# Optimization experiments

Hardware: AMD Instinct MI355X
Metric: run time of the kernel (lower is better)

Reference implementation:

```python
import jax, jax.numpy as jnp
import numpy as np

B, C, H, W = 2, 32, 128, 128
P = 32                      # encoder patch size (== decoder_out_feat_size_final_linear -> empty up_tail)
D = 512                     # encoder dim == decoder dim (enc_to_dec = Identity)
HEADS, DHEAD = 8, 64
ENC_DEPTH = 4
FLIN, CUP = 32, 4
DI, DS, K, DTR, OUTCH = 32, 8, 4, 2, 20   # SS2D dims (c_in=32 hardcoded in module)


def _ln(x, g, b):
    m = x.mean(-1, keepdims=True)
    v = ((x - m) ** 2).mean(-1, keepdims=True)
    return (x - m) / jnp.sqrt(v + 1e-5) * g + b


def _attn(x, g, b, wqkv, wo, bo):
    Bb, N, _ = x.shape
    qkv = _ln(x, g, b) @ wqkv
    q, k, v = jnp.split(qkv, 3, axis=-1)
    sp = lambda t: t.reshape(Bb, N, HEADS, DHEAD).transpose(0, 2, 1, 3)
    q, k, v = sp(q), sp(k), sp(v)
    a = jax.nn.softmax(jnp.einsum('bhnd,bhmd->bhnm', q, k) * (DHEAD ** -0.5), axis=-1)
    o = jnp.einsum('bhnm,bhmd->bhnd', a, v).transpose(0, 2, 1, 3).reshape(Bb, N, HEADS * DHEAD)
    return o @ wo + bo


def _ff(x, g, b, w1, b1, w2, b2):
    return jax.nn.gelu(_ln(x, g, b) @ w1 + b1, approximate=False) @ w2 + b2


def _conv(x, w, b, groups=1):
    y = jax.lax.conv_general_dilated(x, w, (1, 1), 'SAME',
        dimension_numbers=('NCHW', 'OIHW', 'NCHW'), feature_group_count=groups)
    return y + b[None, :, None, None]


def _fft2c(x):
    x = jnp.fft.ifftshift(x, axes=(-2, -1))
    x = jnp.fft.fft2(x, axes=(-2, -1), norm='ortho')
    return jnp.fft.fftshift(x, axes=(-2, -1))


def _ifft2c(x):
    x = jnp.fft.ifftshift(x, axes=(-2, -1))
    x = jnp.fft.ifft2(x, axes=(-2, -1), norm='ortho')
    return jnp.fft.fftshift(x, axes=(-2, -1))


def setup_inputs():
    key = jax.random.key(0)
    it = iter(jax.random.split(key, 80))
    nk = lambda: next(it)
    rn = lambda shape, s=0.02: jax.random.normal(nk(), shape, jnp.float32) * s
    nh, nw = H // P, W // P
    N = nh * nw
    pd = P * P * C
    inp = {}
    inp['in_imgs'] = jax.random.normal(nk(), (B, C, H, W), jnp.float32)
    inp['in_ksp'] = rn((B, C, H, W), 0.01)
    inp['mask'] = (jax.random.uniform(nk(), (B, 1, H, W)) < 0.3).astype(jnp.float32)
    s = jax.random.normal(nk(), (B, C, H, W), jnp.float32)
    sc = s[:, 0::2] + 1j * s[:, 1::2]
    sc = sc / jnp.sqrt(jnp.sum(jnp.abs(sc) ** 2, axis=1, keepdims=True) + 1e-8)
    inp['sens'] = jnp.stack([sc.real, sc.imag], axis=2).reshape(B, C, H, W)
    # patch embedding: LayerNorm(pd) -> Linear(pd, D) -> LayerNorm(D)
    inp['pe_ln1_g'] = jnp.ones((pd,)); inp['pe_ln1_b'] = jnp.zeros((pd,))
    inp['pe_w'] = rn((pd, D)); inp['pe_b'] = jnp.zeros((D,))
    inp['pe_ln2_g'] = jnp.ones((D,)); inp['pe_ln2_b'] = jnp.zeros((D,))
    inp['pos_emb'] = rn((1, N, D))
    dep = ENC_DEPTH
    inp['enc_aln_g'] = jnp.ones((dep, D)); inp['enc_aln_b'] = jnp.zeros((dep, D))
    inp['enc_wqkv'] = rn((dep, D, 3 * HEADS * DHEAD)); inp['enc_wo'] = rn((dep, HEADS * DHEAD, D)); inp['enc_bo'] = jnp.zeros((dep, D))
    inp['enc_fln_g'] = jnp.ones((dep, D)); inp['enc_fln_b'] = jnp.zeros((dep, D))
    inp['enc_w1'] = rn((dep, D, 2048)); inp['enc_b1'] = jnp.zeros((dep, 2048))
    inp['enc_w2'] = rn((dep, 2048, D)); inp['enc_b2'] = jnp.zeros((dep, D))
    inp['enc_ng'] = jnp.ones((D,)); inp['enc_nb'] = jnp.zeros((D,))
    inp['dec_pos'] = rn((N, D))
    inp['dec_aln_g'] = jnp.ones((D,)); inp['dec_aln_b'] = jnp.zeros((D,))
    inp['dec_wqkv'] = rn((D, 3 * HEADS * DHEAD)); inp['dec_wo'] = rn((HEADS * DHEAD, D)); inp['dec_bo'] = jnp.zeros((D,))
    inp['dec_fln_g'] = jnp.ones((D,)); inp['dec_fln_b'] = jnp.zeros((D,))
    inp['dec_w1'] = rn((D, 3072)); inp['dec_b1'] = jnp.zeros((3072,))
    inp['dec_w2'] = rn((3072, D)); inp['dec_b2'] = jnp.zeros((D,))
    inp['dec_ng'] = jnp.ones((D,)); inp['dec_nb'] = jnp.zeros((D,))
    inp['fin_w'] = rn((D, CUP * FLIN * FLIN)); inp['fin_b'] = jnp.zeros((CUP * FLIN * FLIN,))
    # SS2D params
    inp['ss_in_w'] = rn((C, 2 * DI), 0.1); inp['ss_in_b'] = jnp.zeros((2 * DI,))
    inp['ss_conv_w'] = rn((DI, 1, 3, 3), 0.1); inp['ss_conv_b'] = jnp.zeros((DI,))
    inp['ss_xproj'] = rn((K, DI, DTR + 2 * DS), 0.1)
    inp['ss_dt_w'] = rn((K, DTR, DI), 0.5); inp['ss_dt_b'] = rn((K, DI), 0.1)
    inp['ss_Alog'] = jnp.log(jnp.tile(jnp.arange(1, DS + 1, dtype=jnp.float32), (K, DI, 1)))
    inp['ss_D'] = jnp.ones((K, DI))
    inp['ss_ln_g'] = jnp.ones((DI,)); inp['ss_ln_b'] = jnp.zeros((DI,))
    inp['ss_out_w'] = rn((DI, OUTCH), 0.1); inp['ss_out_b'] = jnp.zeros((OUTCH,))
    # RefinementBlock (in_ch = CUP + 32 + OUTCH = 56)
    inp['last_head_w'] = rn((64, CUP + C + OUTCH, 3, 3), 0.05); inp['last_head_b'] = jnp.zeros((64,))
    inp['res_w1'] = rn((3, 64, 64, 3, 3), 0.05); inp['res_b1'] = jnp.zeros((3, 64))
    inp['res_w2'] = rn((3, 64, 64, 3, 3), 0.05); inp['res_b2'] = jnp.zeros((3, 64))
    inp['last_tail_w'] = rn((2, 64, 3, 3), 0.05); inp['last_tail_b'] = jnp.zeros((2,))
    inp['dc_alpha'] = jnp.array(1.0, jnp.float32)
    return inp


def _forward(in_imgs, in_ksp, mask, sens, pe_ln1_g, pe_ln1_b, pe_w, pe_b, pe_ln2_g, pe_ln2_b, pos_emb, enc_aln_g, enc_aln_b, enc_wqkv, enc_wo, enc_bo, enc_fln_g, enc_fln_b, enc_w1, enc_b1, enc_w2, enc_b2, enc_ng, enc_nb, dec_pos, dec_aln_g, dec_aln_b, dec_wqkv, dec_wo, dec_bo, dec_fln_g, dec_fln_b, dec_w1, dec_b1, dec_w2, dec_b2, dec_ng, dec_nb, fin_w, fin_b, ss_in_w, ss_in_b, ss_conv_w, ss_conv_b, ss_xproj, ss_dt_w, ss_dt_b, ss_Alog, ss_D, ss_ln_g, ss_ln_b, ss_out_w, ss_out_b, last_head_w, last_head_b, res_w1, res_b1, res_w2, res_b2, last_tail_w, last_tail_b, dc_alpha):
    nh, nw = H // P, W // P
    N = nh * nw
    # patchify: bb cc (h p1) (w p2) -> bb (h w) (p1 p2 cc)
    pch = in_imgs.reshape(B, C, nh, P, nw, P).transpose(0, 2, 4, 3, 5, 1).reshape(B, N, P * P * C)
    t = _ln(pch, pe_ln1_g, pe_ln1_b) @ pe_w + pe_b
    t = _ln(t, pe_ln2_g, pe_ln2_b)
    t = t + pos_emb   # pool == 'mean'
    for i in range(ENC_DEPTH):
        t = _attn(t, enc_aln_g[i], enc_aln_b[i], enc_wqkv[i], enc_wo[i], enc_bo[i]) + t
        t = _ff(t, enc_fln_g[i], enc_fln_b[i], enc_w1[i], enc_b1[i], enc_w2[i], enc_b2[i]) + t
    t = _ln(t, enc_ng, enc_nb)
    # decoder transformer (depth 1); enc_to_dec is Identity
    d = t + dec_pos[None]
    d = _attn(d, dec_aln_g, dec_aln_b, dec_wqkv, dec_wo, dec_bo) + d
    d = _ff(d, dec_fln_g, dec_fln_b, dec_w1, dec_b1, dec_w2, dec_b2) + d
    d = _ln(d, dec_ng, dec_nb)
    lat = d @ fin_w + fin_b
    # bb (nh nw) (cc p1 p2) -> bb cc (nh p1) (nw p2); up_tail is empty (P == FLIN)
    x = lat.reshape(B, nh, nw, CUP, FLIN, FLIN).transpose(0, 3, 1, 4, 2, 5).reshape(B, CUP, H, W)
    # ---- SS2D: 4-directional selective scan over in_ksp ----
    L = H * W
    xz = jnp.einsum('bchw,ce->behw', in_ksp, ss_in_w) + ss_in_b[None, :, None, None]
    xs0, z = xz[:, :DI], xz[:, DI:]
    xs0 = jax.nn.silu(_conv(xs0, ss_conv_w, ss_conv_b, groups=DI))
    x_hw = xs0.reshape(B, DI, L)
    x_wh = xs0.transpose(0, 1, 3, 2).reshape(B, DI, L)
    xs = jnp.stack([x_hw, x_wh, x_hw[..., ::-1], x_wh[..., ::-1]], axis=1)   # (B,K,DI,L)
    dbl = jnp.einsum('bkdl,kdc->bkcl', xs, ss_xproj)
    dtr, Bm, Cm = dbl[:, :, :DTR], dbl[:, :, DTR:DTR + DS], dbl[:, :, DTR + DS:]
    dts = jax.nn.softplus(jnp.einsum('bkrl,krd->bkdl', dtr, ss_dt_w) + ss_dt_b[None, :, :, None])
    A = -jnp.exp(ss_Alog)
    a = jnp.exp(jnp.einsum('bkdl,kds->bklds', dts, A))         # transition per step
    bb = jnp.einsum('bkdl,bksl->bklds', dts * xs, Bm)          # input per step
    def comb(e1, e2):
        a1, b1 = e1; a2, b2 = e2
        return a1 * a2, a2 * b1 + b2
    _, hs = jax.lax.associative_scan(comb, (a, bb), axis=2)    # (B,K,L,DI,DS)
    ys = jnp.einsum('bklds,bksl->bkdl', hs, Cm) + ss_D[None, :, :, None] * xs
    yh = ys[:, 0] + ys[:, 2, :, ::-1]
    yw = ys[:, 1] + ys[:, 3, :, ::-1]
    y = yh + yw.reshape(B, DI, W, H).transpose(0, 1, 3, 2).reshape(B, DI, L)
    y = y.reshape(B, DI, H, W).transpose(0, 2, 3, 1)           # BHWC
    y = _ln(y, ss_ln_g, ss_ln_b) * jax.nn.silu(z.transpose(0, 2, 3, 1))
    out_ss = (y @ ss_out_w + ss_out_b).transpose(0, 3, 1, 2)   # (B,OUTCH,H,W)
    # ---- refinement ----
    lrelu = lambda v: jnp.where(v > 0, v, 0.2 * v)
    xc = jnp.concatenate([x, in_imgs, out_ss], axis=1)
    h0 = lrelu(_conv(xc, last_head_w, last_head_b))
    for i in range(3):
        h0 = lrelu(h0 + _conv(lrelu(_conv(h0, res_w1[i], res_b1[i])), res_w2[i], res_b2[i]))
    x_ri = _conv(h0, last_tail_w, last_tail_b)   # (B,2,H,W)
    # ---- data consistency ----
    x_c = (x_ri[:, 0] + 1j * x_ri[:, 1])[:, None]
    k_meas = (in_ksp[:, 0::2] + 1j * in_ksp[:, 1::2]) * 100.0   # k_scale_ratio
    s_c = sens[:, 0::2] + 1j * sens[:, 1::2]
    k_pred = _fft2c(s_c * x_c)
    k_dc = k_pred + mask * dc_alpha * (k_meas - k_pred)
    x_comb = jnp.sum(_ifft2c(k_dc) * jnp.conj(s_c), axis=1)
    out_ri = jnp.stack([x_comb.real, x_comb.imag], axis=1)
    return jnp.sqrt(out_ri[:, 0:1] ** 2 + out_ri[:, 1:2] ** 2 + 1e-12)


reference = _forward
```

## Files before the change

kernel.cpp:

```cpp
#include <hip/hip_runtime.h>

#define PI_F 3.14159265358979323846f

constexpr int L_ = 16384;
constexpr int PD_ = 32768;

__device__ __forceinline__ float sigmoidf_(float x){ return 1.f/(1.f+__expf(-x)); }
__device__ __forceinline__ float softplusf_(float x){ return x>20.f ? x : log1pf(__expf(x)); }
__device__ __forceinline__ float geluf_(float x){ return 0.5f*x*(1.f+erff(x*0.70710678118654752f)); }

__device__ __forceinline__ float2 block_reduce2(float s, float ss){
  __shared__ float r1[256], r2[256];
  int tid = threadIdx.x;
  r1[tid]=s; r2[tid]=ss; __syncthreads();
  for(int o=128;o>0;o>>=1){ if(tid<o){ r1[tid]+=r1[tid+o]; r2[tid]+=r2[tid+o]; } __syncthreads(); }
  float2 out; out.x=r1[0]; out.y=r2[0]; __syncthreads();
  return out;
}

__global__ __launch_bounds__(256) void k_pesum(const float* __restrict__ img, float* __restrict__ stats){
  int blk=blockIdx.x; int m=blk>>3, sl=blk&7;
  int b=m>>4, n=m&15, ih=n>>2, iw=n&3;
  int tid=threadIdx.x;
  const float* base=img+(size_t)b*32*L_;
  float s=0.f, ss=0.f;
  for (int i=tid;i<4096;i+=256){
    int j=sl*4096+i;
    int c=j>>10, p1=(j>>5)&31, p2=j&31;
    float v=base[(size_t)c*L_+(ih*32+p1)*128+iw*32+p2];
    s+=v; ss+=v*v;
  }
  float2 r=block_reduce2(s,ss);
  if (tid==0){ atomicAdd(&stats[m*2],r.x); atomicAdd(&stats[m*2+1],r.y); }
}

__global__ __launch_bounds__(256) void k_penorm(const float* __restrict__ img, const float* __restrict__ stats,
                                                const float* __restrict__ g, const float* __restrict__ bv,
                                                float* __restrict__ xn){
  int blk=blockIdx.x; int m=blk>>3, sl=blk&7;
  int b=m>>4, n=m&15, ih=n>>2, iw=n&3;
  int tid=threadIdx.x;
  const float* base=img+(size_t)b*32*L_;
  float mean=stats[m*2]/(float)PD_;
  float var =stats[m*2+1]/(float)PD_-mean*mean;
  float inv =1.f/sqrtf(var+1e-5f);
  for (int i=tid;i<4096;i+=256){
    int j=sl*4096+i;
    int c=j>>10, p1=(j>>5)&31, p2=j&31;
    float v=base[(size_t)c*L_+(ih*32+p1)*128+iw*32+p2];
    int k=(p1*32+p2)*32+c;
    xn[(size_t)m*PD_+k]=(v-mean)*inv*g[k]+bv[k];
  }
}

template<int KC, int MODE>
__global__ __launch_bounds__(256) void k_gemm_sk(const float* __restrict__ A, const float* __restrict__ Bw,
                                                 const float* __restrict__ bias, float* __restrict__ C,
                                                 int N, int K){
  __shared__ float As[32][KC];
  int tid=threadIdx.x, tx=tid&63, ty=tid>>6;
  int n = blockIdx.x*64+tx;
  int k0 = blockIdx.y*KC;
  for (int i=tid;i<32*KC;i+=256){
    int r=i/KC, c=i%KC;
    float v=A[(size_t)r*K + k0 + c];
    if (MODE==1) v=geluf_(v);
    As[r][c]=v;
  }
  __syncthreads();
  float acc[8]={0,0,0,0,0,0,0,0};
  for (int kk=0;kk<KC;kk+=4){
    float b0=Bw[(size_t)(k0+kk)*N+n],   b1=Bw[(size_t)(k0+kk+1)*N+n];
    float b2=Bw[(size_t)(k0+kk+2)*N+n], b3=Bw[(size_t)(k0+kk+3)*N+n];
    #pragma unroll
    for (int r=0;r<8;r++){
      const float4 a=*(const float4*)&As[ty*8+r][kk];
      acc[r]+=a.x*b0+a.y*b1+a.z*b2+a.w*b3;
    }
  }
  bool addb = (bias!=nullptr) && (blockIdx.y==0);
  #pragma unroll
  for (int r=0;r<8;r++){
    int m=ty*8+r;
    float v=acc[r]+(addb?bias[n]:0.f);
    if (MODE==2){
      int b=m>>4, ih=(m>>2)&3, iw=m&3;
      int cu=n>>10, f1=(n>>5)&31, f2=n&31;
      atomicAdd(&C[((size_t)(b*4+cu)*128+ih*32+f1)*128+iw*32+f2], v);
    } else {
      atomicAdd(&C[(size_t)m*N+n], v);
    }
  }
}

__global__ __launch_bounds__(256) void k_pe_post(float* __restrict__ t,
                                                 const float* __restrict__ g, const float* __restrict__ bv,
                                                 const float* __restrict__ pos){
  int m=blockIdx.x, tid=threadIdx.x;
  float v0 = t[m*512+tid];
  float v1 = t[m*512+256+tid];
  float2 r = block_reduce2(v0+v1, v0*v0+v1*v1);
  float mean=r.x/512.f, var=r.y/512.f-mean*mean, inv=1.f/sqrtf(var+1e-5f);
  int n = m&15;
  t[m*512+tid]     = (v0-mean)*inv*g[tid]+bv[tid]         + pos[n*512+tid];
  t[m*512+256+tid] = (v1-mean)*inv*g[256+tid]+bv[256+tid] + pos[n*512+256+tid];
}

__global__ __launch_bounds__(256) void k_ln_tok(const float* __restrict__ src, const float* __restrict__ g,
                                                const float* __restrict__ bv, float* __restrict__ dst){
  int m=blockIdx.x, tid=threadIdx.x;
  float v0=src[m*512+tid], v1=src[m*512+256+tid];
  float2 r=block_reduce2(v0+v1, v0*v0+v1*v1);
  float mean=r.x/512.f, var=r.y/512.f-mean*mean, inv=1.f/sqrtf(var+1e-5f);
  dst[m*512+tid]     =(v0-mean)*inv*g[tid]+bv[tid];
  dst[m*512+256+tid] =(v1-mean)*inv*g[256+tid]+bv[256+tid];
}

__global__ void k_addpos(const float* __restrict__ t, const float* __restrict__ pos, float* __restrict__ dst){
  int i = blockIdx.x*256+threadIdx.x;
  int m=i>>9, j=i&511;
  dst[i]=t[i]+pos[(m&15)*512+j];
}

__global__ __launch_bounds__(256) void k_attn(const float* __restrict__ qkv, float* __restrict__ outb){
  int bh=blockIdx.x, b=bh>>3, h=bh&7, tid=threadIdx.x;
  __shared__ float q[16][64], kk[16][64], vv[16][64], pp[16][16];
  for (int i=tid;i<1024;i+=256){
    int row=i>>6, d=i&63;
    const float* src=qkv + (size_t)(b*16+row)*1536 + h*64+d;
    q[row][d]=src[0]; kk[row][d]=src[512]; vv[row][d]=src[1024];
  }
  __syncthreads();
  int i=tid>>4, j=tid&15;
  float s=0.f;
  #pragma unroll
  for (int d=0;d<64;d++) s+=q[i][d]*kk[j][d];
  s*=0.125f;
  float mx=s;
  for (int o=8;o>0;o>>=1) mx=fmaxf(mx,__shfl_xor(mx,o,16));
  float e=__expf(s-mx), sm=e;
  for (int o=8;o>0;o>>=1) sm+=__shfl_xor(sm,o,16);
  pp[i][j]=e/sm;
  __syncthreads();
  int d=tid&63;
  for (int pass=0;pass<4;pass++){
    int row=pass*4+(tid>>6);
    float acc=0.f;
    #pragma unroll
    for (int jj=0;jj<16;jj++) acc+=pp[row][jj]*vv[jj][d];
    outb[(size_t)(b*16+row)*512 + h*64+d]=acc;
  }
}

__global__ __launch_bounds__(256) void k_xz(const float* __restrict__ ksp, const float* __restrict__ w,
                                            const float* __restrict__ bv, float* __restrict__ xz){
  int blk=blockIdx.x; int b=blk>>6; int p0=(blk&63)*256; int tid=threadIdx.x;
  __shared__ float lin[32][256];
  __shared__ float lw[2048];
  for (int i=tid;i<2048;i+=256) lw[i]=w[i];
  for (int i=tid;i<8192;i+=256){ int c=i>>8, p=i&255; lin[c][p]=ksp[(size_t)(b*32+c)*L_+p0+p]; }
  __syncthreads();
  float xv[32];
  #pragma unroll
  for (int c=0;c<32;c++) xv[c]=lin[c][tid];
  for (int e=0;e<64;e++){
    float a=bv[e];
    #pragma unroll
    for (int c=0;c<32;c++) a+=xv[c]*lw[c*64+e];
    xz[(size_t)(b*64+e)*L_+p0+tid]=a;
  }
}

__global__ void k_dwconv(const float* __restrict__ xz, const float* __restrict__ w,
                         const float* __restrict__ bv, float* __restrict__ xs0){
  int i=blockIdx.x*256+threadIdx.x;
  int p=i&16383; int d=(i>>14)&31; int b=i>>19;
  int h=p>>7, ww=p&127;
  const float* src=xz+(size_t)(b*64+d)*L_;
  float acc=bv[d];
  for (int ky=0;ky<3;ky++){
    int hh=h+ky-1; if(hh<0||hh>127) continue;
    for (int kx=0;kx<3;kx++){
      int wx=ww+kx-1; if(wx<0||wx>127) continue;
      acc+=src[hh*128+wx]*w[d*9+ky*3+kx];
    }
  }
  xs0[(size_t)(b*32+d)*L_+p]=acc*sigmoidf_(acc);
}

__global__ __launch_bounds__(256) void k_transpose(const float* __restrict__ src, float* __restrict__ dst){
  __shared__ float tile[32][33];
  int z=blockIdx.z;
  int h0=blockIdx.y*32, w0=blockIdx.x*32;
  int tid=threadIdx.x, tx=tid&31, ty=tid>>5;
  const float* s=src+(size_t)z*L_;
  float* d=dst+(size_t)z*L_;
  for (int r=ty;r<32;r+=8) tile[r][tx]=s[(h0+r)*128+w0+tx];
  __syncthreads();
  for (int r=ty;r<32;r+=8) d[(w0+r)*128+h0+tx]=tile[tx][r];
}

__global__ __launch_bounds__(256) void k_dbl(const float* __restrict__ xs0, const float* __restrict__ xs0T,
                                             const float* __restrict__ xproj, float* __restrict__ dbl){
  int bk=blockIdx.y; int b=bk>>2, k=bk&3;
  int l0=blockIdx.x*256, tid=threadIdx.x;
  const float* src=(k&1)?xs0T:xs0;
  __shared__ float xv[32][256];
  __shared__ float xp[576];
  for (int i=tid;i<576;i+=256) xp[i]=xproj[k*576+i];
  for (int i=tid;i<8192;i+=256){
    int dd=i>>8, p=i&255; int l=l0+p; int li=(k<2)?l:(16383-l);
    xv[dd][p]=src[(size_t)(b*32+dd)*L_+li];
  }
  __syncthreads();
  float xr[32];
  #pragma unroll
  for (int dd=0;dd<32;dd++) xr[dd]=xv[dd][tid];
  float* out=&dbl[((size_t)(b*4+k)*L_ + l0+tid)*18];
  for (int c=0;c<18;c++){
    float a=0.f;
    #pragma unroll
    for (int dd=0;dd<32;dd++) a+=xr[dd]*xp[dd*18+c];
    out[c]=a;
  }
}

__global__ __launch_bounds__(256) void k_scan1(const float* __restrict__ dbl, const float* __restrict__ xs0,
                                               const float* __restrict__ xs0T, const float* __restrict__ dtw,
                                               const float* __restrict__ dtb, const float* __restrict__ Alog,
                                               float2* __restrict__ sm){
  int blk=blockIdx.x; int bk=blk>>7, c=blk&127;
  int b=bk>>2, k=bk&3;
  int tid=threadIdx.x, d=tid>>3, s=tid&7;
  __shared__ float ed[128][18];
  __shared__ float2 du[32][129];
  const float* dbase=dbl+((size_t)bk*L_+c*128)*18;
  for (int i=tid;i<2304;i+=256) ((float*)ed)[i]=dbase[i];
  __syncthreads();
  const float* src=(k&1)?xs0T:xs0;
  bool rev=(k>=2);
  for (int i=tid;i<4096;i+=256){
    int dd=i>>7, j=i&127; int l=c*128+j;
    float xsv=src[(size_t)(b*32+dd)*L_+(rev?(16383-l):l)];
    float w0=dtw[(k*2+0)*32+dd], w1=dtw[(k*2+1)*32+dd], bb=dtb[k*32+dd];
    float dt=softplusf_(ed[j][0]*w0+ed[j][1]*w1+bb);
    du[dd][j]=make_float2(dt, dt*xsv);
  }
  __syncthreads();
  float Av=-__expf(Alog[(k*32+d)*8+s]);
  float P=1.f, Q=0.f;
  for (int j=0;j<128;j++){
    float2 v=du[d][j];
    float a=__expf(v.x*Av);
    Q=a*Q+v.y*ed[j][2+s];
    P*=a;
  }
  sm[((size_t)bk*128+c)*256+tid]=make_float2(P,Q);
}

__global__ __launch_bounds__(256) void k_scan2(const float2* __restrict__ sm, float* __restrict__ pre){
  int bk=blockIdx.x, tid=threadIdx.x;
  float run=0.f;
  for (int cb=0; cb<128; cb+=16){
    float2 v[16];
    #pragma unroll
    for (int t=0;t<16;t++) v[t]=sm[((size_t)bk*128+cb+t)*256+tid];
    #pragma unroll
    for (int t=0;t<16;t++){
      pre[((size_t)bk*128+cb+t)*256+tid]=run;
      run=v[t].x*run+v[t].y;
    }
  }
}

__global__ __launch_bounds__(256) void k_scan3(const float* __restrict__ dbl, const float* __restrict__ xs0,
                                               const float* __restrict__ xs0T, const float* __restrict__ dtw,
                                               const float* __restrict__ dtb, const float* __restrict__ Alog,
                                               const float* __restrict__ pre, float* __restrict__ ys){
  int blk=blockIdx.x; int bk=blk>>7, c=blk&127;
  int b=bk>>2, k=bk&3;
  int tid=threadIdx.x, d=tid>>3, s=tid&7;
  __shared__ float ed[128][18];
  __shared__ float2 du[32][129];
  const float* dbase=dbl+((size_t)bk*L_+c*128)*18;
  for (int i=tid;i<2304;i+=256) ((float*)ed)[i]=dbase[i];
  __syncthreads();
  const float* src=(k&1)?xs0T:xs0;
  bool rev=(k>=2);
  for (int i=tid;i<4096;i+=256){
    int dd=i>>7, j=i&127; int l=c*128+j;
    float xsv=src[(size_t)(b*32+dd)*L_+(rev?(16383-l):l)];
    float w0=dtw[(k*2+0)*32+dd], w1=dtw[(k*2+1)*32+dd], bb=dtb[k*32+dd];
    float dt=softplusf_(ed[j][0]*w0+ed[j][1]*w1+bb);
    du[dd][j]=make_float2(dt, dt*xsv);
  }
  __syncthreads();
  float Av=-__expf(Alog[(k*32+d)*8+s]);
  float h=pre[((size_t)bk*128+c)*256+tid];
  float* yout=ys+((size_t)bk*32+d)*L_+c*128;
  for (int j=0;j<128;j++){
    float2 v=du[d][j];
    float a=__expf(v.x*Av);
    h=a*h+v.y*ed[j][2+s];
    float yp=h*ed[j][10+s];
    yp+=__shfl_xor(yp,1,8);
    yp+=__shfl_xor(yp,2,8);
    yp+=__shfl_xor(yp,4,8);
    if (s==0) yout[j]=yp;
  }
}

__global__ __launch_bounds__(256) void k_ycomb(const float* __restrict__ ys, const float* __restrict__ xz,
                                               const float* __restrict__ xs0, const float* __restrict__ Dp,
                                               const float* __restrict__ g, const float* __restrict__ bv,
                                               const float* __restrict__ ow, const float* __restrict__ ob,
                                               float* __restrict__ oss){
  int blk=blockIdx.x; int b=blk>>7; int pg=blk&127;
  int tid=threadIdx.x; int pos=tid&127; int team=tid>>7;
  int p=pg*128+pos;
  int lt=pos*128+pg;
  __shared__ float lw[640]; __shared__ float lb[20]; __shared__ float lg[32], lbv[32], lD[32];
  __shared__ float red[2][2][128];
  __shared__ float prj[128][21];
  for (int i=tid;i<640;i+=256) lw[i]=ow[i];
  if (tid<20) lb[tid]=ob[tid];
  if (tid<32){ lg[tid]=g[tid]; lbv[tid]=bv[tid]; lD[tid]=Dp[tid]+Dp[32+tid]+Dp[64+tid]+Dp[96+tid]; }
  __syncthreads();
  size_t base=(size_t)b*128*L_;
  int d0=team*16;
  float y[16];
  float s=0.f, ss=0.f;
  #pragma unroll
  for (int dd=0;dd<16;dd++){
    int d=d0+dd;
    float v=ys[base+(size_t)(0*32+d)*L_+p] + ys[base+(size_t)(2*32+d)*L_+16383-p]
          + ys[base+(size_t)(1*32+d)*L_+lt] + ys[base+(size_t)(3*32+d)*L_+16383-lt]
          + lD[d]*xs0[(size_t)(b*32+d)*L_+p];
    y[dd]=v; s+=v; ss+=v*v;
  }
  red[team][0][pos]=s; red[team][1][pos]=ss;
  __syncthreads();
  float S=red[0][0][pos]+red[1][0][pos];
  float SS=red[0][1][pos]+red[1][1][pos];
  float mean=S/32.f, var=SS/32.f-mean*mean, inv=1.f/sqrtf(var+1e-5f);
  float pc[20];
  #pragma unroll
  for (int c2=0;c2<20;c2++) pc[c2]=0.f;
  #pragma unroll
  for (int dd=0;dd<16;dd++){
    int d=d0+dd;
    float yn=(y[dd]-mean)*inv*lg[d]+lbv[d];
    float zv=xz[(size_t)(b*64+32+d)*L_+p];
    float t2=yn*(zv*sigmoidf_(zv));
    #pragma unroll
    for (int c2=0;c2<20;c2++) pc[c2]+=t2*lw[d*20+c2];
  }
  if (team==1){
    #pragma unroll
    for (int c2=0;c2<20;c2++) prj[pos][c2]=pc[c2];
  }
  __syncthreads();
  if (team==0){
    #pragma unroll
    for (int c2=0;c2<20;c2++) oss[(size_t)(b*20+c2)*L_+p]=lb[c2]+pc[c2]+prj[pos][c2];
  }
}

__global__ void k_concat(const float* __restrict__ x, const float* __restrict__ img,
                         const float* __restrict__ oss, float* __restrict__ xc){
  int i=blockIdx.x*256+threadIdx.x;
  int p=i&16383; int ch=(i>>14)%56; int b=i/(56*16384);
  float v;
  if (ch<4) v=x[(size_t)(b*4+ch)*L_+p];
  else if (ch<36) v=img[(size_t)(b*32+ch-4)*L_+p];
  else v=oss[(size_t)(b*20+ch-36)*L_+p];
  xc[i]=v;
}

template<int NCO>
__global__ __launch_bounds__(256) void k_conv3s(const float* __restrict__ in, const float* __restrict__ wt,
                                                float* __restrict__ sc, int Cin, int Cout, int CIS){
  int tile=blockIdx.x; int th0=(tile>>2)*32, tw0=(tile&3)*32;
  int cg=blockIdx.y;
  int bz=blockIdx.z; int b=bz>>1, ks=bz&1;
  int cibase=ks*CIS;
  int cic=Cin-cibase; if (cic>CIS) cic=CIS;
  __shared__ float wlds[32][NCO][9];
  __shared__ float ibuf[2][34][34];
  int tid=threadIdx.x;
  for (int i=tid;i<cic*NCO*9;i+=256){
    int ci=i/(NCO*9), rem=i%(NCO*9), co=rem/9, q=rem%9;
    wlds[ci][co][q]=wt[(((size_t)(cg*NCO+co))*Cin + cibase+ci)*9+q];
  }
  auto stage=[&](int buf, int ci){
    const float* src=in+((size_t)b*Cin+cibase+ci)*L_;
    for (int i=tid;i<34*34;i+=256){
      int r=i/34, c=i%34;
      int gh=th0+r-1, gw=tw0+c-1;
      ibuf[buf][r][c]=(gh>=0&&gh<128&&gw>=0&&gw<128)?src[gh*128+gw]:0.f;
    }
  };
  stage(0,0);
  __syncthreads();
  float acc[NCO][4];
  #pragma unroll
  for (int co=0;co<NCO;co++){acc[co][0]=0.f;acc[co][1]=0.f;acc[co][2]=0.f;acc[co][3]=0.f;}
  int tr=((tid>>4)&15)<<1, tc=(tid&15)<<1;
  for (int ci=0;ci<cic;ci++){
    int cur=ci&1;
    if (ci+1<cic) stage(cur^1, ci+1);
    float iv[4][4];
    #pragma unroll
    for (int dr=0;dr<4;dr++)
      #pragma unroll
      for (int dc=0;dc<4;dc++) iv[dr][dc]=ibuf[cur][tr+dr][tc+dc];
    #pragma unroll
    for (int co=0;co<NCO;co++){
      float w0=wlds[ci][co][0],w1=wlds[ci][co][1],w2=wlds[ci][co][2];
      float w3=wlds[ci][co][3],w4=wlds[ci][co][4],w5=wlds[ci][co][5];
      float w6=wlds[ci][co][6],w7=wlds[ci][co][7],w8=wlds[ci][co][8];
      acc[co][0]+=iv[0][0]*w0+iv[0][1]*w1+iv[0][2]*w2
                 +iv[1][0]*w3+iv[1][1]*w4+iv[1][2]*w5
                 +iv[2][0]*w6+iv[2][1]*w7+iv[2][2]*w8;
      acc[co][1]+=iv[0][1]*w0+iv[0][2]*w1+iv[0][3]*w2
                 +iv[1][1]*w3+iv[1][2]*w4+iv[1][3]*w5
                 +iv[2][1]*w6+iv[2][2]*w7+iv[2][3]*w8;
      acc[co][2]+=iv[1][0]*w0+iv[1][1]*w1+iv[1][2]*w2
                 +iv[2][0]*w3+iv[2][1]*w4+iv[2][2]*w5
                 +iv[3][0]*w6+iv[3][1]*w7+iv[3][2]*w8;
      acc[co][3]+=iv[1][1]*w0+iv[1][2]*w1+iv[1][3]*w2
                 +iv[2][1]*w3+iv[2][2]*w4+iv[2][3]*w5
                 +iv[3][1]*w6+iv[3][2]*w7+iv[3][3]*w8;
    }
    __syncthreads();
  }
  #pragma unroll
  for (int co=0;co<NCO;co++){
    int gco=cg*NCO+co;
    float* dst=sc+((size_t)((ks*2+b)*Cout+gco))*L_+(size_t)(th0+tr)*128+tw0+tc;
    float2 a={acc[co][0],acc[co][1]}, c={acc[co][2],acc[co][3]};
    *(float2*)dst=a;
    *(float2*)(dst+128)=c;
  }
}

__global__ void k_epi(const float* __restrict__ sc, const float* __restrict__ bias,
                      const float* __restrict__ res, float* __restrict__ out, int Cout, int act){
  int i=blockIdx.x*256+threadIdx.x;
  int co=(i/L_)%Cout;
  size_t half=(size_t)2*Cout*L_;
  float v=sc[i]+sc[half+i]+bias[co];
  if (res) v+=res[i];
  if (act) v=v>0.f?v:0.2f*v;
  out[i]=v;
}

__device__ __forceinline__ int rev7(int x){
  return ((x&1)<<6)|((x&2)<<4)|((x&4)<<2)|(x&8)|((x&16)>>2)|((x&32)>>4)|((x&64)>>6);
}

__global__ __launch_bounds__(256) void k_fftA(const float* __restrict__ x_ri, const float* __restrict__ sens,
                                              float* __restrict__ tmp){
  int blk=blockIdx.x; int b=blk>>7, coil=(blk>>3)&15, rg=blk&7;
  int r0=rg*16;
  __shared__ float Ar[16][128], Ai[16][128];
  __shared__ float twr[64], twi[64];
  int tid=threadIdx.x;
  if (tid<64){ float ang=-2.f*PI_F*(float)tid/128.f; twr[tid]=cosf(ang); twi[tid]=sinf(ang); }
  const float* srp=sens+(size_t)(b*32+2*coil)*L_;
  const float* sip=sens+(size_t)(b*32+2*coil+1)*L_;
  const float* xrp=x_ri+(size_t)(b*2)*L_;
  const float* xip=xrp+L_;
  for (int i=tid;i<2048;i+=256){
    int lr=i>>7, w=i&127; int gh=r0+lr; int idx=gh*128+w;
    float sg=((gh+w)&1)?-1.f:1.f;
    float sr=srp[idx],si=sip[idx],xr=xrp[idx],xi=xip[idx];
    Ar[lr][w]=sg*(sr*xr-si*xi);
    Ai[lr][w]=sg*(sr*xi+si*xr);
  }
  __syncthreads();
  for (int s=0;s<7;s++){
    int m=64>>s;
    for (int q=tid;q<1024;q+=256){
      int lr=q>>6, jj=q&63;
      int j=jj&(m-1), gg=jj>>(6-s);
      int kpos=(gg<<(7-s))+j;
      int tw=j<<s;
      float ur=Ar[lr][kpos],ui=Ai[lr][kpos],vr=Ar[lr][kpos+m],vi=Ai[lr][kpos+m];
      Ar[lr][kpos]=ur+vr; Ai[lr][kpos]=ui+vi;
      float dr=ur-vr,di=ui-vi,wr=twr[tw],wi=twi[tw];
      Ar[lr][kpos+m]=dr*wr-di*wi; Ai[lr][kpos+m]=dr*wi+di*wr;
    }
    __syncthreads();
  }
  float* tr=tmp+(size_t)(b*16+coil)*2*L_;
  float* ti=tr+L_;
  for (int i=tid;i<2048;i+=256){
    int lr=i>>7, w=i&127; int idx=(r0+lr)*128+w;
    tr[idx]=Ar[lr][w]; ti[idx]=Ai[lr][w];
  }
}

__global__ __launch_bounds__(256) void k_fftB(float* __restrict__ tmp, const float* __restrict__ ksp,
                                              const float* __restrict__ mask, const float* __restrict__ alpha_p){
  int blk=blockIdx.x; int b=blk>>7, coil=(blk>>3)&15, cg=blk&7;
  int c0=cg*16;
  __shared__ float Br[128][17], Bi[128][17];
  __shared__ float twr[64], twi[64];
  int tid=threadIdx.x;
  if (tid<64){ float ang=-2.f*PI_F*(float)tid/128.f; twr[tid]=cosf(ang); twi[tid]=sinf(ang); }
  float* tr=tmp+(size_t)(b*16+coil)*2*L_;
  float* ti=tr+L_;
  for (int i=tid;i<2048;i+=256){
    int r=i>>4, lc=i&15;
    Br[r][lc]=tr[r*128+c0+lc]; Bi[r][lc]=ti[r*128+c0+lc];
  }
  __syncthreads();
  for (int s=0;s<7;s++){
    int m=64>>s;
    for (int q=tid;q<1024;q+=256){
      int lc=q&15, jj=q>>4;
      int j=jj&(m-1), gg=jj>>(6-s);
      int kpos=(gg<<(7-s))+j;
      int tw=j<<s;
      float ur=Br[kpos][lc],ui=Bi[kpos][lc],vr=Br[kpos+m][lc],vi=Bi[kpos+m][lc];
      Br[kpos][lc]=ur+vr; Bi[kpos][lc]=ui+vi;
      float dr=ur-vr,di=ui-vi,wr=twr[tw],wi=twi[tw];
      Br[kpos+m][lc]=dr*wr-di*wi; Bi[kpos+m][lc]=dr*wi+di*wr;
    }
    __syncthreads();
  }
  float alpha=alpha_p[0];
  const float* krp=ksp+(size_t)(b*32+2*coil)*L_;
  const float* kip=ksp+(size_t)(b*32+2*coil+1)*L_;
  const float* mkp=mask+(size_t)b*L_;
  for (int i=tid;i<2048;i+=256){
    int r=i>>4, lc=i&15;
    int k1=rev7(r), k2=rev7(c0+lc);
    int kidx=k1*128+k2;
    float mv=mkp[kidx]*alpha;
    float sg=((k1+k2)&1)?-128.f:128.f;
    float kr=krp[kidx]*100.f*sg, ki=kip[kidx]*100.f*sg;
    Br[r][lc]=(1.f-mv)*Br[r][lc]+mv*kr;
    Bi[r][lc]=(1.f-mv)*Bi[r][lc]+mv*ki;
  }
  __syncthreads();
  for (int s=0;s<7;s++){
    int m=1<<s;
    for (int q=tid;q<1024;q+=256){
      int lc=q&15, jj=q>>4;
      int j=jj&(m-1), gg=jj>>s;
      int kpos=(gg<<(s+1))+j;
      int tw=j<<(6-s);
      float wr=twr[tw], wi=-twi[tw];
      float vr=Br[kpos+m][lc],vi=Bi[kpos+m][lc];
      float t2r=vr*wr-vi*wi, t2i=vr*wi+vi*wr;
      float ur=Br[kpos][lc],ui=Bi[kpos][lc];
      Br[kpos][lc]=ur+t2r; Bi[kpos][lc]=ui+t2i;
      Br[kpos+m][lc]=ur-t2r; Bi[kpos+m][lc]=ui-t2i;
    }
    __syncthreads();
  }
  for (int i=tid;i<2048;i+=256){
    int r=i>>4, lc=i&15;
    tr[r*128+c0+lc]=Br[r][lc]; ti[r*128+c0+lc]=Bi[r][lc];
  }
}

__global__ __launch_bounds__(256) void k_fftC(const float* __restrict__ tmp, const float* __restrict__ sens,
                                              float* __restrict__ acc){
  int blk=blockIdx.x; int b=blk>>7, coil=(blk>>3)&15, rg=blk&7;
  int r0=rg*16;
  __shared__ float Ar[16][128], Ai[16][128];
  __shared__ float twr[64], twi[64];
  int tid=threadIdx.x;
  if (tid<64){ float ang=-2.f*PI_F*(float)tid/128.f; twr[tid]=cosf(ang); twi[tid]=sinf(ang); }
  const float* tr=tmp+(size_t)(b*16+coil)*2*L_;
  const float* ti=tr+L_;
  for (int i=tid;i<2048;i+=256){
    int lr=i>>7, w=i&127; int idx=(r0+lr)*128+w;
    Ar[lr][w]=tr[idx]; Ai[lr][w]=ti[idx];
  }
  __syncthreads();
  for (int s=0;s<7;s++){
    int m=1<<s;
    for (int q=tid;q<1024;q+=256){
      int lr=q>>6, jj=q&63;
      int j=jj&(m-1), gg=jj>>s;
      int kpos=(gg<<(s+1))+j;
      int tw=j<<(6-s);
      float wr=twr[tw], wi=-twi[tw];
      float vr=Ar[lr][kpos+m],vi=Ai[lr][kpos+m];
      float t2r=vr*wr-vi*wi, t2i=vr*wi+vi*wr;
      float ur=Ar[lr][kpos],ui=Ai[lr][kpos];
      Ar[lr][kpos]=ur+t2r; Ai[lr][kpos]=ui+t2i;
      Ar[lr][kpos+m]=ur-t2r; Ai[lr][kpos+m]=ui-t2i;
    }
    __syncthreads();
  }
  const float* srp=sens+(size_t)(b*32+2*coil)*L_;
  const float* sip=sens+(size_t)(b*32+2*coil+1)*L_;
  float* accr=acc+(size_t)(b*2)*L_;
  float* acci=accr+L_;
  for (int i=tid;i<2048;i+=256){
    int lr=i>>7, w=i&127; int gh=r0+lr; int idx=gh*128+w;
    float sc=(((gh+w)&1)?-1.f:1.f)*(1.f/16384.f);
    float wr2=Ar[lr][w]*sc, wi2=Ai[lr][w]*sc;
    float sr=srp[idx], si=sip[idx];
    atomicAdd(&accr[idx], sr*wr2+si*wi2);
    atomicAdd(&acci[idx], sr*wi2-si*wr2);
  }
}

__global__ void k_mag(const float* __restrict__ acc, float* __restrict__ out){
  int i=blockIdx.x*256+threadIdx.x;
  int b=i>>14, p=i&16383;
  float re=acc[(size_t)(b*2)*L_+p], im=acc[(size_t)(b*2+1)*L_+p];
  out[i]=sqrtf(re*re+im*im+1e-12f);
}

extern "C" void kernel_launch(void* const* d_in, const int* in_sizes, int n_in,
                              void* d_out, int out_size, void* d_ws, size_t ws_size,
                              hipStream_t stream){
  const float* in_imgs=(const float*)d_in[0];
  const float* in_ksp=(const float*)d_in[1];
  const float* mask=(const float*)d_in[2];
  const float* sens=(const float*)d_in[3];
  const float* pe_ln1_g=(const float*)d_in[4];
  const float* pe_ln1_b=(const float*)d_in[5];
  const float* pe_w=(const float*)d_in[6];
  const float* pe_b=(const float*)d_in[7];
  const float* pe_ln2_g=(const float*)d_in[8];
  const float* pe_ln2_b=(const float*)d_in[9];
  const float* pos_emb=(const float*)d_in[10];
  const float* enc_aln_g=(const float*)d_in[11];
  const float* enc_aln_b=(const float*)d_in[12];
  const float* enc_wqkv=(const float*)d_in[13];
  const float* enc_wo=(const float*)d_in[14];
  const float* enc_bo=(const float*)d_in[15];
  const float* enc_fln_g=(const float*)d_in[16];
  const float* enc_fln_b=(const float*)d_in[17];
  const float* enc_w1=(const float*)d_in[18];
  const float* enc_b1=(const float*)d_in[19];
  const float* enc_w2=(const float*)d_in[20];
  const float* enc_b2=(const float*)d_in[21];
  const float* enc_ng=(const float*)d_in[22];
  const float* enc_nb=(const float*)d_in[23];
  const float* dec_pos=(const float*)d_in[24];
  const float* dec_aln_g=(const float*)d_in[25];
  const float* dec_aln_b=(const float*)d_in[26];
  const float* dec_wqkv=(const float*)d_in[27];
  const float* dec_wo=(const float*)d_in[28];
  const float* dec_bo=(const float*)d_in[29];
  const float* dec_fln_g=(const float*)d_in[30];
  const float* dec_fln_b=(const float*)d_in[31];
  const float* dec_w1=(const float*)d_in[32];
  const float* dec_b1=(const float*)d_in[33];
  const float* dec_w2=(const float*)d_in[34];
  const float* dec_b2=(const float*)d_in[35];
  const float* dec_ng=(const float*)d_in[36];
  const float* dec_nb=(const float*)d_in[37];
  const float* fin_w=(const float*)d_in[38];
  const float* fin_b=(const float*)d_in[39];
  const float* ss_in_w=(const float*)d_in[40];
  const float* ss_in_b=(const float*)d_in[41];
  const float* ss_conv_w=(const float*)d_in[42];
  const float* ss_conv_b=(const float*)d_in[43];
  const float* ss_xproj=(const float*)d_in[44];
  const float* ss_dt_w=(const float*)d_in[45];
  const float* ss_dt_b=(const float*)d_in[46];
  const float* ss_Alog=(const float*)d_in[47];
  const float* ss_D=(const float*)d_in[48];
  const float* ss_ln_g=(const float*)d_in[49];
  const float* ss_ln_b=(const float*)d_in[50];
  const float* ss_out_w=(const float*)d_in[51];
  const float* ss_out_b=(const float*)d_in[52];
  const float* head_w=(const float*)d_in[53];
  const float* head_b=(const float*)d_in[54];
  const float* res_w1=(const float*)d_in[55];
  const float* res_b1=(const float*)d_in[56];
  const float* res_w2=(const float*)d_in[57];
  const float* res_b2=(const float*)d_in[58];
  const float* tail_w=(const float*)d_in[59];
  const float* tail_b=(const float*)d_in[60];
  const float* dc_alpha=(const float*)d_in[61];

  char* ws=(char*)d_ws;
  size_t off=0;
  auto alloc=[&](size_t nfloats)->float*{ float* p=(float*)(ws+off); off+=((nfloats*4+255)/256)*256; return p; };
  float* xn   =alloc((size_t)32*32768);
  float* stats=alloc(64);
  float* tA   =alloc(32*512);
  float* tB   =alloc(32*512);
  float* aln  =alloc(32*512);
  float* qkv  =alloc(32*1536);
  float* attno=alloc(32*512);
  float* ffh  =alloc(32*3072);
  float* xup  =alloc((size_t)2*4*L_);
  float* xz   =alloc((size_t)2*64*L_);
  float* xs0  =alloc((size_t)2*32*L_);
  float* xs0T =alloc((size_t)2*32*L_);
  float* dbl  =alloc((size_t)2*4*L_*18);
  float* ys   =alloc((size_t)2*4*32*L_);
  float* smv  =alloc((size_t)8*128*256*2);
  float* prebuf=alloc((size_t)8*128*256);
  float* oss  =alloc((size_t)2*20*L_);
  float* xc   =alloc((size_t)2*56*L_);
  float* h0   =alloc((size_t)2*64*L_);
  float* tmpc =alloc((size_t)2*64*L_);
  float* csc  =alloc((size_t)2*2*64*L_);
  float* x_ri =alloc((size_t)2*2*L_);
  float* ftmp =alloc((size_t)32*2*L_);
  float* accb =alloc((size_t)2*2*L_);
  (void)ws_size; (void)in_sizes; (void)n_in; (void)out_size;

  hipMemsetAsync(stats, 0, 64*4, stream);
  k_pesum<<<256,256,0,stream>>>(in_imgs, stats);
  k_penorm<<<256,256,0,stream>>>(in_imgs, stats, pe_ln1_g, pe_ln1_b, xn);
  hipMemsetAsync(tA, 0, 32*512*4, stream);
  k_gemm_sk<256,0><<<dim3(8,128),256,0,stream>>>(xn, pe_w, pe_b, tA, 512, 32768);
  k_pe_post<<<32,256,0,stream>>>(tA, pe_ln2_g, pe_ln2_b, pos_emb);

  for (int i=0;i<4;i++){
    k_ln_tok<<<32,256,0,stream>>>(tA, enc_aln_g+i*512, enc_aln_b+i*512, aln);
    hipMemsetAsync(qkv, 0, 32*1536*4, stream);
    k_gemm_sk<64,0><<<dim3(24,8),256,0,stream>>>(aln, enc_wqkv+(size_t)i*512*1536, nullptr, qkv, 1536, 512);
    k_attn<<<16,256,0,stream>>>(qkv, attno);
    k_gemm_sk<64,0><<<dim3(8,8),256,0,stream>>>(attno, enc_wo+(size_t)i*512*512, enc_bo+i*512, tA, 512, 512);
    k_ln_tok<<<32,256,0,stream>>>(tA, enc_fln_g+i*512, enc_fln_b+i*512, aln);
    hipMemsetAsync(ffh, 0, 32*2048*4, stream);
    k_gemm_sk<64,0><<<dim3(32,8),256,0,stream>>>(aln, enc_w1+(size_t)i*512*2048, enc_b1+i*2048, ffh, 2048, 512);
    k_gemm_sk<64,1><<<dim3(8,32),256,0,stream>>>(ffh, enc_w2+(size_t)i*2048*512, enc_b2+i*512, tA, 512, 2048);
  }
  k_ln_tok<<<32,256,0,stream>>>(tA, enc_ng, enc_nb, tA);
  k_addpos<<<64,256,0,stream>>>(tA, dec_pos, tB);
  k_ln_tok<<<32,256,0,stream>>>(tB, dec_aln_g, dec_aln_b, aln);
  hipMemsetAsync(qkv, 0, 32*1536*4, stream);
  k_gemm_sk<64,0><<<dim3(24,8),256,0,stream>>>(aln, dec_wqkv, nullptr, qkv, 1536, 512);
  k_attn<<<16,256,0,stream>>>(qkv, attno);
  k_gemm_sk<64,0><<<dim3(8,8),256,0,stream>>>(attno, dec_wo, dec_bo, tB, 512, 512);
  k_ln_tok<<<32,256,0,stream>>>(tB, dec_fln_g, dec_fln_b, aln);
  hipMemsetAsync(ffh, 0, 32*3072*4, stream);
  k_gemm_sk<64,0><<<dim3(48,8),256,0,stream>>>(aln, dec_w1, dec_b1, ffh, 3072, 512);
  k_gemm_sk<64,1><<<dim3(8,48),256,0,stream>>>(ffh, dec_w2, dec_b2, tB, 512, 3072);
  k_ln_tok<<<32,256,0,stream>>>(tB, dec_ng, dec_nb, tB);
  hipMemsetAsync(xup, 0, (size_t)2*4*L_*4, stream);
  k_gemm_sk<64,2><<<dim3(64,8),256,0,stream>>>(tB, fin_w, fin_b, xup, 4096, 512);

  k_xz<<<128,256,0,stream>>>(in_ksp, ss_in_w, ss_in_b, xz);
  k_dwconv<<<4096,256,0,stream>>>(xz, ss_conv_w, ss_conv_b, xs0);
  k_transpose<<<dim3(4,4,64),256,0,stream>>>(xs0, xs0T);
  k_dbl<<<dim3(64,8),256,0,stream>>>(xs0, xs0T, ss_xproj, dbl);
  k_scan1<<<1024,256,0,stream>>>(dbl, xs0, xs0T, ss_dt_w, ss_dt_b, ss_Alog, (float2*)smv);
  k_scan2<<<8,256,0,stream>>>((const float2*)smv, prebuf);
  k_scan3<<<1024,256,0,stream>>>(dbl, xs0, xs0T, ss_dt_w, ss_dt_b, ss_Alog, prebuf, ys);
  k_ycomb<<<256,256,0,stream>>>(ys, xz, xs0, ss_D, ss_ln_g, ss_ln_b, ss_out_w, ss_out_b, oss);

  k_concat<<<7168,256,0,stream>>>(xup, in_imgs, oss, xc);
  k_conv3s<4><<<dim3(16,16,4),256,0,stream>>>(xc, head_w, csc, 56, 64, 28);
  k_epi<<<8192,256,0,stream>>>(csc, head_b, nullptr, h0, 64, 1);
  for (int i=0;i<3;i++){
    k_conv3s<4><<<dim3(16,16,4),256,0,stream>>>(h0, res_w1+(size_t)i*64*64*9, csc, 64, 64, 32);
    k_epi<<<8192,256,0,stream>>>(csc, res_b1+i*64, nullptr, tmpc, 64, 1);
    k_conv3s<4><<<dim3(16,16,4),256,0,stream>>>(tmpc, res_w2+(size_t)i*64*64*9, csc, 64, 64, 32);
    k_epi<<<8192,256,0,stream>>>(csc, res_b2+i*64, h0, h0, 64, 1);
  }
  k_conv3s<2><<<dim3(16,1,4),256,0,stream>>>(h0, tail_w, csc, 64, 2, 32);
  k_epi<<<256,256,0,stream>>>(csc, tail_b, nullptr, x_ri, 2, 0);

  hipMemsetAsync(accb, 0, (size_t)2*2*L_*4, stream);
  k_fftA<<<256,256,0,stream>>>(x_ri, sens, ftmp);
  k_fftB<<<256,256,0,stream>>>(ftmp, in_ksp, mask, dc_alpha);
  k_fftC<<<256,256,0,stream>>>(ftmp, sens, accb);
  k_mag<<<128,256,0,stream>>>(accb, (float*)d_out);
}
```

Baseline: 1.582 ms.

## Fold memsets into preceding kernels, widen conv tiles, vectorize epilogue

Removes the separate hipMemsetAsync calls by adding extra blocks to the preceding LayerNorm, penorm and epilogue kernels that zero the next split-K accumulation buffer. The 3x3 conv tile grows to 32x64 with 2x4 outputs per thread and float4 LDS reads and global stores, halving the block count. The conv epilogue now works on float4 elements. This trims launch and memset overhead and raises per-thread reuse in the conv, at the cost of more registers per thread and fewer blocks to spread across the GPU.

```diff
diff --git a/kernel.cpp b/kernel.cpp
--- a/kernel.cpp
+++ b/kernel.cpp
@@ -36,8 +36,14 @@
 
 __global__ __launch_bounds__(256) void k_penorm(const float* __restrict__ img, const float* __restrict__ stats,
                                                 const float* __restrict__ g, const float* __restrict__ bv,
-                                                float* __restrict__ xn){
-  int blk=blockIdx.x; int m=blk>>3, sl=blk&7;
+                                                float* __restrict__ xn, float4* __restrict__ zbuf, int zn4){
+  int blk=blockIdx.x;
+  if (blk>=256){
+    int i=(blk-256)*256+threadIdx.x;
+    if (i<zn4) zbuf[i]=make_float4(0.f,0.f,0.f,0.f);
+    return;
+  }
+  int m=blk>>3, sl=blk&7;
   int b=m>>4, n=m&15, ih=n>>2, iw=n&3;
   int tid=threadIdx.x;
   const float* base=img+(size_t)b*32*L_;
@@ -106,9 +112,16 @@
   t[m*512+256+tid] = (v1-mean)*inv*g[256+tid]+bv[256+tid] + pos[n*512+256+tid];
 }
 
-__global__ __launch_bounds__(256) void k_ln_tok(const float* __restrict__ src, const float* __restrict__ g,
-                                                const float* __restrict__ bv, float* __restrict__ dst){
-  int m=blockIdx.x, tid=threadIdx.x;
+__global__ __launch_bounds__(256) void k_ln_tokz(const float* __restrict__ src, const float* __restrict__ g,
+                                                 const float* __restrict__ bv, float* __restrict__ dst,
+                                                 float4* __restrict__ zbuf, int zn4){
+  int blk=blockIdx.x;
+  if (blk>=32){
+    int i=(blk-32)*256+threadIdx.x;
+    if (i<zn4) zbuf[i]=make_float4(0.f,0.f,0.f,0.f);
+    return;
+  }
+  int m=blk, tid=threadIdx.x;
   float v0=src[m*512+tid], v1=src[m*512+256+tid];
   float2 r=block_reduce2(v0+v1, v0*v0+v1*v1);
   float mean=r.x/512.f, var=r.y/512.f-mean*mean, inv=1.f/sqrtf(var+1e-5f);
@@ -378,15 +391,15 @@
 }
 
 template<int NCO>
-__global__ __launch_bounds__(256) void k_conv3s(const float* __restrict__ in, const float* __restrict__ wt,
+__global__ __launch_bounds__(256) void k_conv3v(const float* __restrict__ in, const float* __restrict__ wt,
                                                 float* __restrict__ sc, int Cin, int Cout, int CIS){
-  int tile=blockIdx.x; int th0=(tile>>2)*32, tw0=(tile&3)*32;
+  int tile=blockIdx.x; int th0=(tile>>1)*32, tw0=(tile&1)*64;
   int cg=blockIdx.y;
   int bz=blockIdx.z; int b=bz>>1, ks=bz&1;
   int cibase=ks*CIS;
   int cic=Cin-cibase; if (cic>CIS) cic=CIS;
   __shared__ float wlds[32][NCO][9];
-  __shared__ float ibuf[2][34][34];
+  __shared__ float ibuf[2][34][68];
   int tid=threadIdx.x;
   for (int i=tid;i<cic*NCO*9;i+=256){
     int ci=i/(NCO*9), rem=i%(NCO*9), co=rem/9, q=rem%9;
@@ -394,43 +407,42 @@
   }
   auto stage=[&](int buf, int ci){
     const float* src=in+((size_t)b*Cin+cibase+ci)*L_;
-    for (int i=tid;i<34*34;i+=256){
-      int r=i/34, c=i%34;
+    for (int i=tid;i<34*66;i+=256){
+      int r=i/66, c=i%66;
       int gh=th0+r-1, gw=tw0+c-1;
       ibuf[buf][r][c]=(gh>=0&&gh<128&&gw>=0&&gw<128)?src[gh*128+gw]:0.f;
     }
   };
   stage(0,0);
   __syncthreads();
-  float acc[NCO][4];
-  #pragma unroll
-  for (int co=0;co<NCO;co++){acc[co][0]=0.f;acc[co][1]=0.f;acc[co][2]=0.f;acc[co][3]=0.f;}
-  int tr=((tid>>4)&15)<<1, tc=(tid&15)<<1;
+  float acc[NCO][8];
+  #pragma unroll
+  for (int co=0;co<NCO;co++)
+    #pragma unroll
+    for (int p2=0;p2<8;p2++) acc[co][p2]=0.f;
+  int tr=2*(tid>>4), tc=4*(tid&15);
   for (int ci=0;ci<cic;ci++){
     int cur=ci&1;
     if (ci+1<cic) stage(cur^1, ci+1);
-    float iv[4][4];
-    #pragma unroll
-    for (int dr=0;dr<4;dr++)
+    float iv[4][8];
+    #pragma unroll
+    for (int r2=0;r2<4;r2++){
+      *(float4*)&iv[r2][0]=*(const float4*)&ibuf[cur][tr+r2][tc];
+      *(float4*)&iv[r2][4]=*(const float4*)&ibuf[cur][tr+r2][tc+4];
+    }
+    #pragma unroll
+    for (int co=0;co<NCO;co++){
+      const float* wp=wlds[ci][co];
+      float w0=wp[0],w1=wp[1],w2=wp[2],w3=wp[3],w4=wp[4],w5=wp[5],w6=wp[6],w7=wp[7],w8=wp[8];
       #pragma unroll
-      for (int dc=0;dc<4;dc++) iv[dr][dc]=ibuf[cur][tr+dr][tc+dc];
-    #pragma unroll
-    for (int co=0;co<NCO;co++){
-      float w0=wlds[ci][co][0],w1=wlds[ci][co][1],w2=wlds[ci][co][2];
-      float w3=wlds[ci][co][3],w4=wlds[ci][co][4],w5=wlds[ci][co][5];
-      float w6=wlds[ci][co][6],w7=wlds[ci][co][7],w8=wlds[ci][co][8];
-      acc[co][0]+=iv[0][0]*w0+iv[0][1]*w1+iv[0][2]*w2
-                 +iv[1][0]*w3+iv[1][1]*w4+iv[1][2]*w5
-                 +iv[2][0]*w6+iv[2][1]*w7+iv[2][2]*w8;
-      acc[co][1]+=iv[0][1]*w0+iv[0][2]*w1+iv[0][3]*w2
-                 +iv[1][1]*w3+iv[1][2]*w4+iv[1][3]*w5
-                 +iv[2][1]*w6+iv[2][2]*w7+iv[2][3]*w8;
-      acc[co][2]+=iv[1][0]*w0+iv[1][1]*w1+iv[1][2]*w2
-                 +iv[2][0]*w3+iv[2][1]*w4+iv[2][2]*w5
-                 +iv[3][0]*w6+iv[3][1]*w7+iv[3][2]*w8;
-      acc[co][3]+=iv[1][1]*w0+iv[1][2]*w1+iv[1][3]*w2
-                 +iv[2][1]*w3+iv[2][2]*w4+iv[2][3]*w5
-                 +iv[3][1]*w6+iv[3][2]*w7+iv[3][3]*w8;
+      for (int pr=0;pr<2;pr++){
+        #pragma unroll
+        for (int pc2=0;pc2<4;pc2++){
+          acc[co][pr*4+pc2]+= iv[pr][pc2]*w0+iv[pr][pc2+1]*w1+iv[pr][pc2+2]*w2
+                             +iv[pr+1][pc2]*w3+iv[pr+1][pc2+1]*w4+iv[pr+1][pc2+2]*w5
+                             +iv[pr+2][pc2]*w6+iv[pr+2][pc2+1]*w7+iv[pr+2][pc2+2]*w8;
+        }
+      }
     }
     __syncthreads();
   }
@@ -438,21 +450,34 @@
   for (int co=0;co<NCO;co++){
     int gco=cg*NCO+co;
     float* dst=sc+((size_t)((ks*2+b)*Cout+gco))*L_+(size_t)(th0+tr)*128+tw0+tc;
-    float2 a={acc[co][0],acc[co][1]}, c={acc[co][2],acc[co][3]};
-    *(float2*)dst=a;
-    *(float2*)(dst+128)=c;
-  }
-}
-
-__global__ void k_epi(const float* __restrict__ sc, const float* __restrict__ bias,
-                      const float* __restrict__ res, float* __restrict__ out, int Cout, int act){
+    float4 a={acc[co][0],acc[co][1],acc[co][2],acc[co][3]};
+    float4 c2={acc[co][4],acc[co][5],acc[co][6],acc[co][7]};
+    *(float4*)dst=a;
+    *(float4*)(dst+128)=c2;
+  }
+}
+
+__global__ void k_epi4(const float4* __restrict__ sc, const float* __restrict__ bias,
+                       const float4* __restrict__ res, float4* __restrict__ out, int Cout, int act,
+                       float4* __restrict__ zbuf, int zn4){
+  int n=2*Cout*4096;
   int i=blockIdx.x*256+threadIdx.x;
-  int co=(i/L_)%Cout;
-  size_t half=(size_t)2*Cout*L_;
-  float v=sc[i]+sc[half+i]+bias[co];
-  if (res) v+=res[i];
-  if (act) v=v>0.f?v:0.2f*v;
-  out[i]=v;
+  if (i>=n){
+    int z=i-n;
+    if (z<zn4) zbuf[z]=make_float4(0.f,0.f,0.f,0.f);
+    return;
+  }
+  int co=(i>>12)%Cout;
+  float4 v=sc[i], w2=sc[(size_t)n+i];
+  float bb=bias[co];
+  float4 r;
+  r.x=v.x+w2.x+bb; r.y=v.y+w2.y+bb; r.z=v.z+w2.z+bb; r.w=v.w+w2.w+bb;
+  if (res){ float4 q=res[i]; r.x+=q.x; r.y+=q.y; r.z+=q.z; r.w+=q.w; }
+  if (act){
+    r.x=r.x>0.f?r.x:0.2f*r.x; r.y=r.y>0.f?r.y:0.2f*r.y;
+    r.z=r.z>0.f?r.z:0.2f*r.z; r.w=r.w>0.f?r.w:0.2f*r.w;
+  }
+  out[i]=r;
 }
 
 __device__ __forceinline__ int rev7(int x){
@@ -716,35 +741,29 @@
 
   hipMemsetAsync(stats, 0, 64*4, stream);
   k_pesum<<<256,256,0,stream>>>(in_imgs, stats);
-  k_penorm<<<256,256,0,stream>>>(in_imgs, stats, pe_ln1_g, pe_ln1_b, xn);
-  hipMemsetAsync(tA, 0, 32*512*4, stream);
+  k_penorm<<<272,256,0,stream>>>(in_imgs, stats, pe_ln1_g, pe_ln1_b, xn, (float4*)tA, 4096);
   k_gemm_sk<256,0><<<dim3(8,128),256,0,stream>>>(xn, pe_w, pe_b, tA, 512, 32768);
   k_pe_post<<<32,256,0,stream>>>(tA, pe_ln2_g, pe_ln2_b, pos_emb);
 
   for (int i=0;i<4;i++){
-    k_ln_tok<<<32,256,0,stream>>>(tA, enc_aln_g+i*512, enc_aln_b+i*512, aln);
-    hipMemsetAsync(qkv, 0, 32*1536*4, stream);
+    k_ln_tokz<<<80,256,0,stream>>>(tA, enc_aln_g+i*512, enc_aln_b+i*512, aln, (float4*)qkv, 12288);
     k_gemm_sk<64,0><<<dim3(24,8),256,0,stream>>>(aln, enc_wqkv+(size_t)i*512*1536, nullptr, qkv, 1536, 512);
     k_attn<<<16,256,0,stream>>>(qkv, attno);
     k_gemm_sk<64,0><<<dim3(8,8),256,0,stream>>>(attno, enc_wo+(size_t)i*512*512, enc_bo+i*512, tA, 512, 512);
-    k_ln_tok<<<32,256,0,stream>>>(tA, enc_fln_g+i*512, enc_fln_b+i*512, aln);
-    hipMemsetAsync(ffh, 0, 32*2048*4, stream);
+    k_ln_tokz<<<96,256,0,stream>>>(tA, enc_fln_g+i*512, enc_fln_b+i*512, aln, (float4*)ffh, 16384);
     k_gemm_sk<64,0><<<dim3(32,8),256,0,stream>>>(aln, enc_w1+(size_t)i*512*2048, enc_b1+i*2048, ffh, 2048, 512);
     k_gemm_sk<64,1><<<dim3(8,32),256,0,stream>>>(ffh, enc_w2+(size_t)i*2048*512, enc_b2+i*512, tA, 512, 2048);
   }
-  k_ln_tok<<<32,256,0,stream>>>(tA, enc_ng, enc_nb, tA);
+  k_ln_tokz<<<32,256,0,stream>>>(tA, enc_ng, enc_nb, tA, nullptr, 0);
   k_addpos<<<64,256,0,stream>>>(tA, dec_pos, tB);
-  k_ln_tok<<<32,256,0,stream>>>(tB, dec_aln_g, dec_aln_b, aln);
-  hipMemsetAsync(qkv, 0, 32*1536*4, stream);
+  k_ln_tokz<<<80,256,0,stream>>>(tB, dec_aln_g, dec_aln_b, aln, (float4*)qkv, 12288);
   k_gemm_sk<64,0><<<dim3(24,8),256,0,stream>>>(aln, dec_wqkv, nullptr, qkv, 1536, 512);
   k_attn<<<16,256,0,stream>>>(qkv, attno);
   k_gemm_sk<64,0><<<dim3(8,8),256,0,stream>>>(attno, dec_wo, dec_bo, tB, 512, 512);
-  k_ln_tok<<<32,256,0,stream>>>(tB, dec_fln_g, dec_fln_b, aln);
-  hipMemsetAsync(ffh, 0, 32*3072*4, stream);
+  k_ln_tokz<<<128,256,0,stream>>>(tB, dec_fln_g, dec_fln_b, aln, (float4*)ffh, 24576);
   k_gemm_sk<64,0><<<dim3(48,8),256,0,stream>>>(aln, dec_w1, dec_b1, ffh, 3072, 512);
   k_gemm_sk<64,1><<<dim3(8,48),256,0,stream>>>(ffh, dec_w2, dec_b2, tB, 512, 3072);
-  k_ln_tok<<<32,256,0,stream>>>(tB, dec_ng, dec_nb, tB);
-  hipMemsetAsync(xup, 0, (size_t)2*4*L_*4, stream);
+  k_ln_tokz<<<160,256,0,stream>>>(tB, dec_ng, dec_nb, tB, (float4*)xup, 32768);
   k_gemm_sk<64,2><<<dim3(64,8),256,0,stream>>>(tB, fin_w, fin_b, xup, 4096, 512);
 
   k_xz<<<128,256,0,stream>>>(in_ksp, ss_in_w, ss_in_b, xz);
@@ -757,18 +776,17 @@
   k_ycomb<<<256,256,0,stream>>>(ys, xz, xs0, ss_D, ss_ln_g, ss_ln_b, ss_out_w, ss_out_b, oss);
 
   k_concat<<<7168,256,0,stream>>>(xup, in_imgs, oss, xc);
-  k_conv3s<4><<<dim3(16,16,4),256,0,stream>>>(xc, head_w, csc, 56, 64, 28);
-  k_epi<<<8192,256,0,stream>>>(csc, head_b, nullptr, h0, 64, 1);
+  k_conv3v<4><<<dim3(8,16,4),256,0,stream>>>(xc, head_w, csc, 56, 64, 28);
+  k_epi4<<<2048,256,0,stream>>>((const float4*)csc, head_b, nullptr, (float4*)h0, 64, 1, nullptr, 0);
   for (int i=0;i<3;i++){
-    k_conv3s<4><<<dim3(16,16,4),256,0,stream>>>(h0, res_w1+(size_t)i*64*64*9, csc, 64, 64, 32);
-    k_epi<<<8192,256,0,stream>>>(csc, res_b1+i*64, nullptr, tmpc, 64, 1);
-    k_conv3s<4><<<dim3(16,16,4),256,0,stream>>>(tmpc, res_w2+(size_t)i*64*64*9, csc, 64, 64, 32);
-    k_epi<<<8192,256,0,stream>>>(csc, res_b2+i*64, h0, h0, 64, 1);
-  }
-  k_conv3s<2><<<dim3(16,1,4),256,0,stream>>>(h0, tail_w, csc, 64, 2, 32);
-  k_epi<<<256,256,0,stream>>>(csc, tail_b, nullptr, x_ri, 2, 0);
-
-  hipMemsetAsync(accb, 0, (size_t)2*2*L_*4, stream);
+    k_conv3v<4><<<dim3(8,16,4),256,0,stream>>>(h0, res_w1+(size_t)i*64*64*9, csc, 64, 64, 32);
+    k_epi4<<<2048,256,0,stream>>>((const float4*)csc, res_b1+i*64, nullptr, (float4*)tmpc, 64, 1, nullptr, 0);
+    k_conv3v<4><<<dim3(8,16,4),256,0,stream>>>(tmpc, res_w2+(size_t)i*64*64*9, csc, 64, 64, 32);
+    k_epi4<<<2048,256,0,stream>>>((const float4*)csc, res_b2+i*64, (const float4*)h0, (float4*)h0, 64, 1, nullptr, 0);
+  }
+  k_conv3v<2><<<dim3(8,1,4),256,0,stream>>>(h0, tail_w, csc, 64, 2, 32);
+  k_epi4<<<128,256,0,stream>>>((const float4*)csc, tail_b, nullptr, (float4*)x_ri, 2, 0, (float4*)accb, 16384);
+
   k_fftA<<<256,256,0,stream>>>(x_ri, sens, ftmp);
   k_fftB<<<256,256,0,stream>>>(ftmp, in_ksp, mask, dc_alpha);
   k_fftC<<<256,256,0,stream>>>(ftmp, sens, accb);
```

Measured after the change: 1.911 ms. 20.8% more time.
